# Kernel tuning notes

Hardware: AMD Instinct MI355X
Metric: run time of the kernel (lower is better)

Reference implementation:

```python
import jax, jax.numpy as jnp
import numpy as np

DIM = 512
N = 131072


def _linear_params(key, dim):
    # torch nn.Linear default init: U(-1/sqrt(in), 1/sqrt(in)) for W and b
    kw, kb = jax.random.split(key)
    bound = 1.0 / np.sqrt(dim)
    W = jax.random.uniform(kw, (dim, dim), jnp.float32, -bound, bound)
    b = jax.random.uniform(kb, (dim,), jnp.float32, -bound, bound)
    return W, b


def setup_inputs() -> dict:
    key = jax.random.key(0)
    ks = jax.random.split(key, 8)
    x = jax.random.normal(ks[0], (N, DIM), jnp.float32)
    h = jax.random.normal(ks[1], (N, DIM), jnp.float32)
    W_rx, b_rx = _linear_params(ks[2], DIM)
    W_rh, b_rh = _linear_params(ks[3], DIM)
    W_zx, b_zx = _linear_params(ks[4], DIM)
    W_zh, b_zh = _linear_params(ks[5], DIM)
    W_nx, b_nx = _linear_params(ks[6], DIM)
    W_nh, b_nh = _linear_params(ks[7], DIM)
    return {
        "x": x, "h": h,
        "W_rx": W_rx, "b_rx": b_rx, "W_rh": W_rh, "b_rh": b_rh,
        "W_zx": W_zx, "b_zx": b_zx, "W_zh": W_zh, "b_zh": b_zh,
        "W_nx": W_nx, "b_nx": b_nx, "W_nh": W_nh, "b_nh": b_nh,
    }


def reference(x, h, W_rx, b_rx, W_rh, b_rh, W_zx, b_zx, W_zh, b_zh,
              W_nx, b_nx, W_nh, b_nh):
    # torch Linear: y = x @ W.T + b  (W stored [out, in])
    r = jax.nn.sigmoid(x @ W_rx.T + b_rx + h @ W_rh.T + b_rh)
    z = jax.nn.sigmoid(x @ W_zx.T + b_zx + h @ W_zh.T + b_zh)
    n = jnp.tanh(x @ W_nx.T + b_nx + (r * h) @ W_nh.T + b_nh)
    return (1.0 - z) * n + z * h
```

## Files before the change

### kernel.cpp

```cpp
#include <hip/hip_runtime.h>

#define DIM 512
#define NROWS 131072

typedef __attribute__((ext_vector_type(8))) __bf16 bf16x8;
typedef __attribute__((ext_vector_type(4))) float f32x4;

__device__ __forceinline__ unsigned short f2bf(float f) {
  unsigned u = __builtin_bit_cast(unsigned, f);
  return (unsigned short)((u + 0x7FFFu + ((u >> 16) & 1u)) >> 16);
}
__device__ __forceinline__ float bf2f(unsigned short u) {
  return __builtin_bit_cast(float, (unsigned)u << 16);
}

__device__ __forceinline__ f32x4 mfma16(bf16x8 a, bf16x8 b, f32x4 c) {
  return __builtin_amdgcn_mfma_f32_16x16x32_bf16(a, b, c, 0, 0, 0);
}

__device__ __forceinline__ float sigmoid_fast(float v) {
  return 1.0f / (1.0f + __expf(-v));
}
__device__ __forceinline__ float tanh_fast(float v) {
  float e = __expf(2.0f * v);
  return 1.0f - 2.0f / (e + 1.0f);
}

__device__ __forceinline__ void gl2lds(const void* g, void* l) {
  __builtin_amdgcn_global_load_lds(
      (const __attribute__((address_space(1))) unsigned int*)g,
      (__attribute__((address_space(3))) unsigned int*)l, 16, 0, 0);
}

__global__ void prepack_weights(const float* __restrict__ W0, const float* __restrict__ W1,
                                const float* __restrict__ W2, const float* __restrict__ W3,
                                const float* __restrict__ W4, const float* __restrict__ W5,
                                unsigned short* __restrict__ out) {
  int idx = blockIdx.x * 256 + threadIdx.x;
  int e = idx & 7;
  int l = (idx >> 3) & 63;
  int c = (idx >> 9) & 31;
  int f = (idx >> 14) & 15;
  int g = idx >> 18;
  const float* W = (g == 0) ? W0 : (g == 1) ? W1 : (g == 2) ? W2
                 : (g == 3) ? W3 : (g == 4) ? W4 : W5;
  int row = c * 16 + (l & 15);
  int kk  = f * 32 + ((l >> 4) << 3) + e;
  out[idx] = f2bf(W[row * DIM + kk]);
}

__global__ void prep_x(const float* __restrict__ x, unsigned short* __restrict__ xb) {
  size_t i = (size_t)(blockIdx.x * 256 + threadIdx.x) * 8;
  float4 a0 = *(const float4*)(x + i);
  float4 a1 = *(const float4*)(x + i + 4);
  union { unsigned short us[8]; uint4 v; } p;
  p.us[0] = f2bf(a0.x); p.us[1] = f2bf(a0.y); p.us[2] = f2bf(a0.z); p.us[3] = f2bf(a0.w);
  p.us[4] = f2bf(a1.x); p.us[5] = f2bf(a1.y); p.us[6] = f2bf(a1.z); p.us[7] = f2bf(a1.w);
  *(uint4*)(xb + i) = p.v;
}

#define BOFF 65536
#define XOFF 131072
#define LDS_BYTES 147456

__global__ __launch_bounds__(512, 1)
void gru_fused(const float* __restrict__ x, const float* __restrict__ h,
               const unsigned short* __restrict__ xb,
               const unsigned char* __restrict__ WB,
               const float* __restrict__ b_rx, const float* __restrict__ b_rh,
               const float* __restrict__ b_zx, const float* __restrict__ b_zh,
               const float* __restrict__ b_nx, const float* __restrict__ b_nh,
               float* __restrict__ out) {
  __shared__ __align__(1024) unsigned char lds[LDS_BYTES];

  const int tid  = threadIdx.x;
  const int lane = tid & 63;
  const int w    = tid >> 6;
  const int cfg0 = w * 4;
  const int row0 = blockIdx.x * 64;
  const int lr   = lane & 15;
  const int lk   = lane >> 4;

  auto stageB = [&](int g, int f, int dst) {
    const unsigned char* src = WB + (size_t)(g * 16 + f) * 32768;
#pragma unroll
    for (int it = 0; it < 4; ++it) {
      int o = (it * 512 + tid) * 16;
      gl2lds(src + o, &lds[dst + o]);
    }
  };
  auto stageXpair = [&](int p) {
    int fh = tid >> 8, rf = (tid >> 6) & 3, l = tid & 63;
    const unsigned short* src = xb + (size_t)(row0 + rf * 16 + (l & 15)) * DIM
                                + p * 64 + fh * 32 + (l >> 4) * 8;
    gl2lds(src, &lds[XOFF + (p & 1) * 8192 + tid * 16]);
  };
  auto gateStage = [&](int abase, int bbase, f32x4 (&A)[4][4]) {
    bf16x8 af[4], bfr[4];
#pragma unroll
    for (int rf = 0; rf < 4; ++rf)
      af[rf] = *(const bf16x8*)&lds[abase + rf * 1024 + lane * 16];
#pragma unroll
    for (int cf = 0; cf < 4; ++cf)
      bfr[cf] = *(const bf16x8*)&lds[bbase + (cfg0 + cf) * 1024 + lane * 16];
#pragma unroll
    for (int rf = 0; rf < 4; ++rf)
#pragma unroll
      for (int cf = 0; cf < 4; ++cf)
        A[rf][cf] = mfma16(af[rf], bfr[cf], A[rf][cf]);
  };

  f32x4 accR[4][4] = {}, accZ[4][4] = {};

#pragma unroll
  for (int it = 0; it < 16; ++it) {
    int i = tid + it * 512;
    int row = i >> 7;
    int k = (i & 127) * 4;
    float4 hv4 = *(const float4*)(h + (size_t)(row0 + row) * DIM + k);
    union { unsigned short us[4]; uint2 v; } p;
    p.us[0] = f2bf(hv4.x); p.us[1] = f2bf(hv4.y);
    p.us[2] = f2bf(hv4.z); p.us[3] = f2bf(hv4.w);
    *(uint2*)&lds[(k >> 5) * 4096 + (row >> 4) * 1024
                  + (((k >> 3) & 3) * 16 + (row & 15)) * 16 + (k & 4) * 2] = p.v;
  }
  stageXpair(0);
  stageB(0, 0, BOFF);
  __syncthreads();

#pragma unroll 1
  for (int f = 0; f < 16; ++f) {
    const int xo = XOFF + ((f >> 1) & 1) * 8192 + (f & 1) * 4096;
    const int ho = f * 4096;
    stageB(1, f, BOFF + 32768);
    if (f & 1) {
      int p1 = (f >> 1) + 1; if (p1 > 7) p1 = 7;
      stageXpair(p1);
      asm volatile("s_waitcnt vmcnt(5)" ::: "memory");
    } else {
      asm volatile("s_waitcnt vmcnt(4)" ::: "memory");
    }
    __builtin_amdgcn_s_barrier();
    gateStage(xo, BOFF, accR);
    __builtin_amdgcn_s_barrier();
    stageB(2, f, BOFF);
    asm volatile("s_waitcnt vmcnt(4)" ::: "memory");
    __builtin_amdgcn_s_barrier();
    gateStage(xo, BOFF + 32768, accZ);
    __builtin_amdgcn_s_barrier();
    stageB(3, f, BOFF + 32768);
    asm volatile("s_waitcnt vmcnt(4)" ::: "memory");
    __builtin_amdgcn_s_barrier();
    gateStage(ho, BOFF, accR);
    __builtin_amdgcn_s_barrier();
    if (f < 15) {
      stageB(0, f + 1, BOFF);
      asm volatile("s_waitcnt vmcnt(4)" ::: "memory");
    } else {
      asm volatile("s_waitcnt vmcnt(0)" ::: "memory");
    }
    __builtin_amdgcn_s_barrier();
    gateStage(ho, BOFF + 32768, accZ);
    __builtin_amdgcn_s_barrier();
  }

#pragma unroll
  for (int cf = 0; cf < 4; ++cf) {
    const int col  = (cfg0 + cf) * 16 + lr;
    const float bs = b_rx[col] + b_rh[col];
    const int fcol  = col >> 5;
    const int l2b   = ((col >> 3) & 3) * 16;
    const int ebyte = (col & 7) * 2;
#pragma unroll
    for (int rf = 0; rf < 4; ++rf) {
#pragma unroll
      for (int j = 0; j < 4; ++j) {
        const int rsub = lk * 4 + j;
        unsigned short hu = *(const unsigned short*)
            &lds[fcol * 4096 + rf * 1024 + (l2b + rsub) * 16 + ebyte];
        float rv = sigmoid_fast(accR[rf][cf][j] + bs);
        *(unsigned short*)
            &lds[BOFF + fcol * 4096 + rf * 1024 + (l2b + rsub) * 16 + ebyte]
            = f2bf(rv * bf2f(hu));
      }
    }
  }
  __syncthreads();

  f32x4 accN[4][4] = {};
  stageXpair(0);
  stageB(4, 0, 0);
#pragma unroll 1
  for (int f = 0; f < 16; ++f) {
    const int xo = XOFF + ((f >> 1) & 1) * 8192 + (f & 1) * 4096;
    stageB(5, f, 32768);
    if (f & 1) {
      int p1 = (f >> 1) + 1; if (p1 > 7) p1 = 7;
      stageXpair(p1);
      asm volatile("s_waitcnt vmcnt(5)" ::: "memory");
    } else {
      asm volatile("s_waitcnt vmcnt(4)" ::: "memory");
    }
    __builtin_amdgcn_s_barrier();
    gateStage(xo, 0, accN);
    __builtin_amdgcn_s_barrier();
    if (f < 15) {
      stageB(4, f + 1, 0);
      asm volatile("s_waitcnt vmcnt(4)" ::: "memory");
    } else {
      asm volatile("s_waitcnt vmcnt(0)" ::: "memory");
    }
    __builtin_amdgcn_s_barrier();
    gateStage(BOFF + f * 4096, 32768, accN);
    __builtin_amdgcn_s_barrier();
  }

#pragma unroll
  for (int cf = 0; cf < 4; ++cf) {
    const int col  = (cfg0 + cf) * 16 + lr;
    const float bn = b_nx[col] + b_nh[col];
    const float bz = b_zx[col] + b_zh[col];
#pragma unroll
    for (int rf = 0; rf < 4; ++rf) {
#pragma unroll
      for (int j = 0; j < 4; ++j) {
        const int row = rf * 16 + lk * 4 + j;
        const size_t off = (size_t)(row0 + row) * DIM + col;
        float hv = h[off];
        float nv = tanh_fast(accN[rf][cf][j] + bn);
        float zv = sigmoid_fast(accZ[rf][cf][j] + bz);
        out[off] = (1.0f - zv) * nv + zv * hv;
      }
    }
  }
}

extern "C" void kernel_launch(void* const* d_in, const int* in_sizes, int n_in,
                              void* d_out, int out_size, void* d_ws, size_t ws_size,
                              hipStream_t stream) {
  const float* x    = (const float*)d_in[0];
  const float* h    = (const float*)d_in[1];
  const float* W_rx = (const float*)d_in[2];
  const float* b_rx = (const float*)d_in[3];
  const float* W_rh = (const float*)d_in[4];
  const float* b_rh = (const float*)d_in[5];
  const float* W_zx = (const float*)d_in[6];
  const float* b_zx = (const float*)d_in[7];
  const float* W_zh = (const float*)d_in[8];
  const float* b_zh = (const float*)d_in[9];
  const float* W_nx = (const float*)d_in[10];
  const float* b_nx = (const float*)d_in[11];
  const float* W_nh = (const float*)d_in[12];
  const float* b_nh = (const float*)d_in[13];

  unsigned char* ws = (unsigned char*)d_ws;
  unsigned short* wpack = (unsigned short*)ws;
  unsigned short* xb    = (unsigned short*)(ws + (4ull << 20));

  prepack_weights<<<6144, 256, 0, stream>>>(W_rx, W_zx, W_rh, W_zh, W_nx, W_nh, wpack);
  prep_x<<<32768, 256, 0, stream>>>(x, xb);
  gru_fused<<<NROWS / 64, 512, 0, stream>>>(x, h, xb, (const unsigned char*)wpack,
                                            b_rx, b_rh, b_zx, b_zh, b_nx, b_nh,
                                            (float*)d_out);
}
```

Baseline: 671.1 us.

## Pre-pack h to bf16 fragment layout and load via async LDS copies

Adds a prep_h kernel that converts h to bf16 in the MFMA fragment order, so the fused kernel can fill its h tile with global_load_lds instead of converting fp32 in-kernel. It also writes r*h in place over the h tile, moves the n-gate weight staging to BOFF, and shares A fragments across the R and Z MFMA stages so they are not read twice from LDS. The change costs an extra pass over h (a 256MB read plus a 128MB write), and it depends on workspace being large enough, with a fallback to the old path otherwise.

```diff
diff --git a/kernel.cpp b/kernel.cpp
--- a/kernel.cpp
+++ b/kernel.cpp
@@ -13,11 +13,9 @@
 __device__ __forceinline__ float bf2f(unsigned short u) {
   return __builtin_bit_cast(float, (unsigned)u << 16);
 }
-
 __device__ __forceinline__ f32x4 mfma16(bf16x8 a, bf16x8 b, f32x4 c) {
   return __builtin_amdgcn_mfma_f32_16x16x32_bf16(a, b, c, 0, 0, 0);
 }
-
 __device__ __forceinline__ float sigmoid_fast(float v) {
   return 1.0f / (1.0f + __expf(-v));
 }
@@ -25,7 +23,6 @@
   float e = __expf(2.0f * v);
   return 1.0f - 2.0f / (e + 1.0f);
 }
-
 __device__ __forceinline__ void gl2lds(const void* g, void* l) {
   __builtin_amdgcn_global_load_lds(
       (const __attribute__((address_space(1))) unsigned int*)g,
@@ -59,13 +56,33 @@
   *(uint4*)(xb + i) = p.v;
 }
 
+__global__ void prep_h(const float* __restrict__ h, unsigned short* __restrict__ hfb) {
+  size_t idx  = (size_t)(blockIdx.x * 256 + threadIdx.x);
+  size_t base = idx * 8;
+  size_t panel = base >> 15;
+  int rem  = (int)(base & 32767);
+  int f    = rem >> 11;
+  int rf   = (rem >> 9) & 3;
+  int lane = (rem >> 3) & 63;
+  int row  = (int)panel * 64 + rf * 16 + (lane & 15);
+  int k    = f * 32 + (lane >> 4) * 8;
+  const float* src = h + (size_t)row * DIM + k;
+  float4 a0 = *(const float4*)src;
+  float4 a1 = *(const float4*)(src + 4);
+  union { unsigned short us[8]; uint4 v; } p;
+  p.us[0] = f2bf(a0.x); p.us[1] = f2bf(a0.y); p.us[2] = f2bf(a0.z); p.us[3] = f2bf(a0.w);
+  p.us[4] = f2bf(a1.x); p.us[5] = f2bf(a1.y); p.us[6] = f2bf(a1.z); p.us[7] = f2bf(a1.w);
+  *(uint4*)(hfb + base) = p.v;
+}
+
 #define BOFF 65536
 #define XOFF 131072
 #define LDS_BYTES 147456
 
 __global__ __launch_bounds__(512, 1)
-void gru_fused(const float* __restrict__ x, const float* __restrict__ h,
+void gru_fused(const float* __restrict__ h,
                const unsigned short* __restrict__ xb,
+               const unsigned short* __restrict__ hfb,
                const unsigned char* __restrict__ WB,
                const float* __restrict__ b_rx, const float* __restrict__ b_rh,
                const float* __restrict__ b_zx, const float* __restrict__ b_zh,
@@ -81,6 +98,8 @@
   const int lr   = lane & 15;
   const int lk   = lane >> 4;
 
+  bf16x8 af[4], bfr[4];
+
   auto stageB = [&](int g, int f, int dst) {
     const unsigned char* src = WB + (size_t)(g * 16 + f) * 32768;
 #pragma unroll
@@ -95,34 +114,48 @@
                                 + p * 64 + fh * 32 + (l >> 4) * 8;
     gl2lds(src, &lds[XOFF + (p & 1) * 8192 + tid * 16]);
   };
-  auto gateStage = [&](int abase, int bbase, f32x4 (&A)[4][4]) {
-    bf16x8 af[4], bfr[4];
+  auto readA4 = [&](int abase) {
 #pragma unroll
     for (int rf = 0; rf < 4; ++rf)
       af[rf] = *(const bf16x8*)&lds[abase + rf * 1024 + lane * 16];
+  };
+  auto readB4 = [&](int bbase) {
 #pragma unroll
     for (int cf = 0; cf < 4; ++cf)
       bfr[cf] = *(const bf16x8*)&lds[bbase + (cfg0 + cf) * 1024 + lane * 16];
-#pragma unroll
-    for (int rf = 0; rf < 4; ++rf)
-#pragma unroll
-      for (int cf = 0; cf < 4; ++cf)
-        A[rf][cf] = mfma16(af[rf], bfr[cf], A[rf][cf]);
   };
 
+#define DOMFMA(ACC)                                                            \
+  do {                                                                         \
+    _Pragma("unroll")                                                          \
+    for (int rf_ = 0; rf_ < 4; ++rf_)                                          \
+      _Pragma("unroll")                                                        \
+      for (int cf_ = 0; cf_ < 4; ++cf_)                                        \
+        ACC[rf_][cf_] = mfma16(af[rf_], bfr[cf_], ACC[rf_][cf_]);              \
+  } while (0)
+
   f32x4 accR[4][4] = {}, accZ[4][4] = {};
 
-#pragma unroll
-  for (int it = 0; it < 16; ++it) {
-    int i = tid + it * 512;
-    int row = i >> 7;
-    int k = (i & 127) * 4;
-    float4 hv4 = *(const float4*)(h + (size_t)(row0 + row) * DIM + k);
-    union { unsigned short us[4]; uint2 v; } p;
-    p.us[0] = f2bf(hv4.x); p.us[1] = f2bf(hv4.y);
-    p.us[2] = f2bf(hv4.z); p.us[3] = f2bf(hv4.w);
-    *(uint2*)&lds[(k >> 5) * 4096 + (row >> 4) * 1024
-                  + (((k >> 3) & 3) * 16 + (row & 15)) * 16 + (k & 4) * 2] = p.v;
+  if (hfb) {
+    const unsigned char* src = (const unsigned char*)(hfb + (size_t)blockIdx.x * 32768);
+#pragma unroll
+    for (int it = 0; it < 8; ++it) {
+      int o = (it * 512 + tid) * 16;
+      gl2lds(src + o, &lds[o]);
+    }
+  } else {
+#pragma unroll
+    for (int it = 0; it < 16; ++it) {
+      int i = tid + it * 512;
+      int row = i >> 7;
+      int k = (i & 127) * 4;
+      float4 hv4 = *(const float4*)(h + (size_t)(row0 + row) * DIM + k);
+      union { unsigned short us[4]; uint2 v; } p;
+      p.us[0] = f2bf(hv4.x); p.us[1] = f2bf(hv4.y);
+      p.us[2] = f2bf(hv4.z); p.us[3] = f2bf(hv4.w);
+      *(uint2*)&lds[(k >> 5) * 4096 + (row >> 4) * 1024
+                    + (((k >> 3) & 3) * 16 + (row & 15)) * 16 + (k & 4) * 2] = p.v;
+    }
   }
   stageXpair(0);
   stageB(0, 0, BOFF);
@@ -141,17 +174,22 @@
       asm volatile("s_waitcnt vmcnt(4)" ::: "memory");
     }
     __builtin_amdgcn_s_barrier();
-    gateStage(xo, BOFF, accR);
+    readA4(xo);
+    readB4(BOFF);
+    DOMFMA(accR);
     __builtin_amdgcn_s_barrier();
     stageB(2, f, BOFF);
     asm volatile("s_waitcnt vmcnt(4)" ::: "memory");
     __builtin_amdgcn_s_barrier();
-    gateStage(xo, BOFF + 32768, accZ);
+    readB4(BOFF + 32768);
+    DOMFMA(accZ);
     __builtin_amdgcn_s_barrier();
     stageB(3, f, BOFF + 32768);
     asm volatile("s_waitcnt vmcnt(4)" ::: "memory");
     __builtin_amdgcn_s_barrier();
-    gateStage(ho, BOFF, accR);
+    readA4(ho);
+    readB4(BOFF);
+    DOMFMA(accR);
     __builtin_amdgcn_s_barrier();
     if (f < 15) {
       stageB(0, f + 1, BOFF);
@@ -160,7 +198,8 @@
       asm volatile("s_waitcnt vmcnt(0)" ::: "memory");
     }
     __builtin_amdgcn_s_barrier();
-    gateStage(ho, BOFF + 32768, accZ);
+    readB4(BOFF + 32768);
+    DOMFMA(accZ);
     __builtin_amdgcn_s_barrier();
   }
 
@@ -176,12 +215,10 @@
 #pragma unroll
       for (int j = 0; j < 4; ++j) {
         const int rsub = lk * 4 + j;
-        unsigned short hu = *(const unsigned short*)
-            &lds[fcol * 4096 + rf * 1024 + (l2b + rsub) * 16 + ebyte];
+        const int addr = fcol * 4096 + rf * 1024 + (l2b + rsub) * 16 + ebyte;
+        unsigned short hu = *(const unsigned short*)&lds[addr];
         float rv = sigmoid_fast(accR[rf][cf][j] + bs);
-        *(unsigned short*)
-            &lds[BOFF + fcol * 4096 + rf * 1024 + (l2b + rsub) * 16 + ebyte]
-            = f2bf(rv * bf2f(hu));
+        *(unsigned short*)&lds[addr] = f2bf(rv * bf2f(hu));
       }
     }
   }
@@ -189,11 +226,11 @@
 
   f32x4 accN[4][4] = {};
   stageXpair(0);
-  stageB(4, 0, 0);
+  stageB(4, 0, BOFF);
 #pragma unroll 1
   for (int f = 0; f < 16; ++f) {
     const int xo = XOFF + ((f >> 1) & 1) * 8192 + (f & 1) * 4096;
-    stageB(5, f, 32768);
+    stageB(5, f, BOFF + 32768);
     if (f & 1) {
       int p1 = (f >> 1) + 1; if (p1 > 7) p1 = 7;
       stageXpair(p1);
@@ -202,16 +239,20 @@
       asm volatile("s_waitcnt vmcnt(4)" ::: "memory");
     }
     __builtin_amdgcn_s_barrier();
-    gateStage(xo, 0, accN);
+    readA4(xo);
+    readB4(BOFF);
+    DOMFMA(accN);
     __builtin_amdgcn_s_barrier();
     if (f < 15) {
-      stageB(4, f + 1, 0);
+      stageB(4, f + 1, BOFF);
       asm volatile("s_waitcnt vmcnt(4)" ::: "memory");
     } else {
       asm volatile("s_waitcnt vmcnt(0)" ::: "memory");
     }
     __builtin_amdgcn_s_barrier();
-    gateStage(BOFF + f * 4096, 32768, accN);
+    readA4(f * 4096);
+    readB4(BOFF + 32768);
+    DOMFMA(accN);
     __builtin_amdgcn_s_barrier();
   }
 
@@ -233,6 +274,7 @@
       }
     }
   }
+#undef DOMFMA
 }
 
 extern "C" void kernel_launch(void* const* d_in, const int* in_sizes, int n_in,
@@ -255,11 +297,17 @@
 
   unsigned char* ws = (unsigned char*)d_ws;
   unsigned short* wpack = (unsigned short*)ws;
-  unsigned short* xb    = (unsigned short*)(ws + (4ull << 20));
+  const size_t SEG = (size_t)NROWS * DIM * 2;
+  unsigned short* xb = (unsigned short*)(ws + (4ull << 20));
+  const size_t hfb_off = (4ull << 20) + SEG;
+  unsigned short* hfb = (ws_size >= hfb_off + SEG)
+                        ? (unsigned short*)(ws + hfb_off)
+                        : (unsigned short*)nullptr;
 
   prepack_weights<<<6144, 256, 0, stream>>>(W_rx, W_zx, W_rh, W_zh, W_nx, W_nh, wpack);
   prep_x<<<32768, 256, 0, stream>>>(x, xb);
-  gru_fused<<<NROWS / 64, 512, 0, stream>>>(x, h, xb, (const unsigned char*)wpack,
+  if (hfb) prep_h<<<32768, 256, 0, stream>>>(h, hfb);
+  gru_fused<<<NROWS / 64, 512, 0, stream>>>(h, xb, hfb, (const unsigned char*)wpack,
                                             b_rx, b_rh, b_zx, b_zh, b_nx, b_nh,
                                             (float*)d_out);
 }
```

Measured after the change: 722.8 us. 1.08x slower.
